# Performance work log

Measured on AMD Instinct MI355X. Metric: run time of the kernel, lower is better.

The kernel has to match this reference:

```python
import jax, jax.numpy as jnp
import numpy as np

NUM_HEADS = 8
EPS = 1e-5


def setup_inputs() -> dict:
    key = jax.random.key(0)
    ks = jax.random.split(key, 7)
    B, C, H, W, D = 1, 256, 16, 16, 16
    return {
        "x": jax.random.normal(ks[0], (B, C, H, W, D), dtype=jnp.float32),
        "w_dw": jax.random.normal(ks[1], (C, 1, 3, 3, 3), dtype=jnp.float32) * 0.05,
        "b_dw": jax.random.normal(ks[2], (C,), dtype=jnp.float32) * 0.05,
        "w_qkv": jax.random.normal(ks[3], (3 * C, C), dtype=jnp.float32) * 0.05,
        "b_qkv": jax.random.normal(ks[4], (3 * C,), dtype=jnp.float32) * 0.05,
        "w_proj": jax.random.normal(ks[5], (C, C), dtype=jnp.float32) * 0.05,
        "b_proj": jax.random.normal(ks[6], (C,), dtype=jnp.float32) * 0.05,
    }


def reference(x, w_dw, b_dw, w_qkv, b_qkv, w_proj, b_proj):
    B, C, H, W, D = x.shape
    nh = NUM_HEADS
    hd = C // nh
    scale = hd ** (-0.5)
    N = H * W * D

    # depthwise 3x3x3 conv (groups=C), SAME padding
    y = jax.lax.conv_general_dilated(
        x, w_dw, window_strides=(1, 1, 1), padding="SAME",
        dimension_numbers=("NCHWD", "OIHWD", "NCHWD"),
        feature_group_count=C,
    ) + b_dw[None, :, None, None, None]

    # InstanceNorm3d (affine=False): normalize over spatial dims per (b, c)
    mu = y.mean(axis=(2, 3, 4), keepdims=True)
    var = y.var(axis=(2, 3, 4), keepdims=True)
    y = (y - mu) * jax.lax.rsqrt(var + EPS)

    # 1x1x1 conv -> 3*C channels
    qkv = jnp.einsum("bchwd,oc->bohwd", y, w_qkv) + b_qkv[None, :, None, None, None]

    # [B, 3, nh, hd, N] -> q, k, v each [B, nh, N, hd]
    qkv = qkv.reshape(B, 3, nh, hd, N)
    q, k, v = jnp.transpose(qkv, (1, 0, 2, 4, 3))

    attn = jax.nn.softmax(jnp.einsum("bhnd,bhmd->bhnm", q, k) * scale, axis=-1)
    out = jnp.einsum("bhnm,bhmd->bhnd", attn, v)  # [B, nh, N, hd]

    # transpose(-1, -2) then reshape to [B, C, H, W, D]
    out = jnp.transpose(out, (0, 1, 3, 2)).reshape(B, C, H, W, D)

    # output 1x1x1 projection
    out = jnp.einsum("bchwd,oc->bohwd", out, w_proj) + b_proj[None, :, None, None, None]
    return out
```

## Files before the change

### kernel.cpp

```cpp
#include <hip/hip_runtime.h>
#include <hip/hip_bf16.h>

#define NSP 4096
#define QSC2 0.25503486f

typedef __attribute__((ext_vector_type(8))) short bf16x8;
typedef __attribute__((ext_vector_type(4))) float f32x4;

__device__ __forceinline__ unsigned short f2bf(float f){
  union{float f;unsigned int u;}c; c.f=f;
  unsigned int r = c.u + 0x7fffu + ((c.u>>16)&1u);
  return (unsigned short)(r>>16);
}
__device__ __forceinline__ unsigned int pk2(float a, float b){
  __hip_bfloat162 p = __float22bfloat162_rn(make_float2(a, b));
  unsigned int r; __builtin_memcpy(&r, &p, 4); return r;
}
__device__ __forceinline__ ushort4 pk4(float a, float b, float c, float d){
  union { ushort4 u4; uint2 u2; } u;
  u.u2.x = pk2(a, b); u.u2.y = pk2(c, d);
  return u.u4;
}

__global__ __launch_bounds__(512) void k_dwconv(
    const float* __restrict__ x,
    const float* __restrict__ wdw,
    const float* __restrict__ bdw,
    unsigned short* __restrict__ ybn)
{
  const int c = blockIdx.x;
  const int tid = threadIdx.x;
  __shared__ float xs[4096];
  __shared__ float wsh[27];
  __shared__ float bsh;
  __shared__ float rs[8], rq[8];

  const float* xc = x + (size_t)c * NSP;
  for (int i = tid; i < 1024; i += 512) *(float4*)&xs[i*4] = ((const float4*)xc)[i];
  if (tid < 27) wsh[tid] = wdw[c*27 + tid];
  if (tid == 31) bsh = bdw[c];
  __syncthreads();

  float yv[8];
  float sum = 0.f, sumsq = 0.f;
  #pragma unroll
  for (int i = 0; i < 8; i++){
    const int n = (i << 9) + tid;
    const int h = n >> 8, w = (n >> 4) & 15, d = n & 15;
    float acc = bsh;
    #pragma unroll
    for (int kh = 0; kh < 3; kh++){
      const int hh = h + kh - 1;
      if ((unsigned)hh >= 16u) continue;
      #pragma unroll
      for (int kw = 0; kw < 3; kw++){
        const int ww = w + kw - 1;
        if ((unsigned)ww >= 16u) continue;
        #pragma unroll
        for (int kd = 0; kd < 3; kd++){
          const int dd = d + kd - 1;
          if ((unsigned)dd >= 16u) continue;
          acc += wsh[kh*9 + kw*3 + kd] * xs[(hh<<8) + (ww<<4) + dd];
        }
      }
    }
    yv[i] = acc; sum += acc; sumsq += acc*acc;
  }
  #pragma unroll
  for (int off = 32; off > 0; off >>= 1){
    sum   += __shfl_down(sum, off, 64);
    sumsq += __shfl_down(sumsq, off, 64);
  }
  const int wid = tid >> 6, lane = tid & 63;
  if (lane == 0){ rs[wid] = sum; rq[wid] = sumsq; }
  __syncthreads();
  float ts = 0.f, tq = 0.f;
  #pragma unroll
  for (int i = 0; i < 8; i++){ ts += rs[i]; tq += rq[i]; }
  const float mean = ts * (1.f/4096.f);
  const float var  = tq * (1.f/4096.f) - mean*mean;
  const float rinv = rsqrtf(var + 1e-5f);
  unsigned short* yo = ybn + (size_t)c * NSP;
  #pragma unroll
  for (int i = 0; i < 8; i++) yo[(i<<9) + tid] = f2bf((yv[i] - mean) * rinv);
}

__global__ __launch_bounds__(256) void k_trans(
    const unsigned short* __restrict__ ybn,
    unsigned short* __restrict__ ynT)
{
  __shared__ unsigned short T[64][72];
  const int tid = threadIdx.x;
  const int n0 = blockIdx.x * 64, c0 = blockIdx.y * 64;
  const int cl = tid >> 4, n4 = (tid & 15) * 4;
  #pragma unroll
  for (int i = 0; i < 4; i++){
    const int c = cl + i*16;
    const ushort4 v = *(const ushort4*)(ybn + (size_t)(c0 + c) * NSP + n0 + n4);
    T[n4+0][c] = v.x; T[n4+1][c] = v.y; T[n4+2][c] = v.z; T[n4+3][c] = v.w;
  }
  __syncthreads();
  const int nl = tid >> 2, s8 = (tid & 3) * 16;
  *(uint4*)(ynT + (size_t)(n0+nl)*256 + c0 + s8)     = *(const uint4*)&T[nl][s8];
  *(uint4*)(ynT + (size_t)(n0+nl)*256 + c0 + s8 + 8) = *(const uint4*)&T[nl][s8 + 8];
}

__global__ __launch_bounds__(256) void k_qkv(
    const float* __restrict__ wqkv,
    const float* __restrict__ bqkv,
    const unsigned short* __restrict__ ynT,
    unsigned short* __restrict__ qb, unsigned short* __restrict__ kb,
    unsigned short* __restrict__ vbt)
{
  __shared__ unsigned short Wb[64][264];
  const int tid = threadIdx.x;
  const int o0 = blockIdx.y * 64;
  const int n0 = blockIdx.x * 128;
  {
    const int row = tid & 63, part = tid >> 6;
    const float* src = wqkv + (size_t)(o0 + row) * 256 + part * 64;
    unsigned short* dst = &Wb[row][part*64];
    #pragma unroll
    for (int j = 0; j < 8; j++){
      const float4 a = ((const float4*)src)[2*j];
      const float4 b = ((const float4*)src)[2*j+1];
      *(ushort4*)&dst[j*8]     = pk4(a.x, a.y, a.z, a.w);
      *(ushort4*)&dst[j*8 + 4] = pk4(b.x, b.y, b.z, b.w);
    }
  }
  __syncthreads();

  const int w = tid >> 6, lane = tid & 63, quad = lane >> 4, cc = lane & 15;
  const int nbase = n0 + w*32;
  const bool isv = (o0 >= 512);
  f32x4 acc[2][4] = {};

  #pragma unroll
  for (int k = 0; k < 8; k++){
    const bf16x8 y0 = *(const bf16x8*)(ynT + (size_t)(nbase + cc)  * 256 + k*32 + quad*8);
    const bf16x8 y1 = *(const bf16x8*)(ynT + (size_t)(nbase+16+cc) * 256 + k*32 + quad*8);
    #pragma unroll
    for (int os = 0; os < 4; os++){
      const bf16x8 wf = *(const bf16x8*)&Wb[os*16 + cc][k*32 + quad*8];
      if (!isv){
        acc[0][os] = __builtin_amdgcn_mfma_f32_16x16x32_bf16(y0, wf, acc[0][os], 0, 0, 0);
        acc[1][os] = __builtin_amdgcn_mfma_f32_16x16x32_bf16(y1, wf, acc[1][os], 0, 0, 0);
      } else {
        acc[0][os] = __builtin_amdgcn_mfma_f32_16x16x32_bf16(wf, y0, acc[0][os], 0, 0, 0);
        acc[1][os] = __builtin_amdgcn_mfma_f32_16x16x32_bf16(wf, y1, acc[1][os], 0, 0, 0);
      }
    }
  }

  if (!isv){
    #pragma unroll
    for (int os = 0; os < 4; os++){
      const int o = o0 + os*16 + cc;
      const int g = o >> 8, hh = (o >> 5) & 7, dd = o & 31;
      const float bias = bqkv[o];
      const float sc = (g == 0) ? QSC2 : 1.f;
      unsigned short* dst = (g == 0) ? qb : kb;
      #pragma unroll
      for (int ns = 0; ns < 2; ns++){
        #pragma unroll
        for (int r = 0; r < 4; r++){
          const int n = nbase + ns*16 + quad*4 + r;
          dst[((size_t)hh * NSP + n) * 32 + dd] = f2bf((acc[ns][os][r] + bias) * sc);
        }
      }
    }
  } else {
    #pragma unroll
    for (int os = 0; os < 4; os++){
      #pragma unroll
      for (int r = 0; r < 4; r++){
        const int orow = o0 - 512 + os*16 + quad*4 + r;
        const float bias = bqkv[512 + orow];
        #pragma unroll
        for (int ns = 0; ns < 2; ns++){
          const int n = nbase + ns*16 + cc;
          vbt[(size_t)orow * NSP + n] = f2bf(acc[ns][os][r] + bias);
        }
      }
    }
  }
}

__global__ __launch_bounds__(256) void k_attn(
    const unsigned short* __restrict__ qb,
    const unsigned short* __restrict__ kb,
    const unsigned short* __restrict__ vbt,
    float* __restrict__ op, float* __restrict__ lp)
{
  const int h = blockIdx.y, q0 = blockIdx.x * 64, z = blockIdx.z;
  const int tid = threadIdx.x;
  const int w = tid >> 6, lane = tid & 63, quad = lane >> 4, cc = lane & 15;

  __shared__ unsigned short ks [128][40];
  __shared__ unsigned short vsT[32][136];
  __shared__ unsigned short pst[64][136];

  const bf16x8 qf = *(const bf16x8*)(qb + ((size_t)(h * NSP + q0 + w*16 + cc)) * 32 + quad*8);
  const unsigned short* kbase = kb  + (size_t)h * NSP * 32;
  const unsigned short* vbase = vbt + (size_t)h * 32 * NSP;

  f32x4 o0 = {0.f,0.f,0.f,0.f}, o1 = {0.f,0.f,0.f,0.f};
  float lsum = 0.f;

  const int kt0 = z << 11;
  const int krow = tid >> 1, kseg = (tid & 1) * 16;
  const int vd = tid >> 3,  vseg = (tid & 7) * 16;

  for (int it = 0; it < 16; it++){
    const int kt = kt0 + it * 128;
    {
      const uint4* src = (const uint4*)(kbase + (size_t)(kt + krow) * 32 + kseg);
      const uint4 a = src[0], b = src[1];
      *(uint4*)&ks[krow][kseg]     = a;
      *(uint4*)&ks[krow][kseg + 8] = b;
    }
    {
      const uint4* src = (const uint4*)(vbase + (size_t)vd * NSP + kt + vseg);
      const uint4 a = src[0], b = src[1];
      *(uint4*)&vsT[vd][vseg]     = a;
      *(uint4*)&vsT[vd][vseg + 8] = b;
    }
    __syncthreads();

    #pragma unroll
    for (int t = 0; t < 8; t++){
      const bf16x8 kf = *(const bf16x8*)&ks[t*16 + cc][quad*8];
      f32x4 a = {0.f,0.f,0.f,0.f};
      a = __builtin_amdgcn_mfma_f32_16x16x32_bf16(kf, qf, a, 0, 0, 0);
      const float p0 = exp2f(a.x), p1 = exp2f(a.y);
      const float p2 = exp2f(a.z), p3 = exp2f(a.w);
      lsum += (p0 + p1) + (p2 + p3);
      *(ushort4*)&pst[w*16 + cc][t*16 + quad*4] = pk4(p0, p1, p2, p3);
    }
    #pragma unroll
    for (int ch = 0; ch < 4; ch++){
      const bf16x8 pf = *(const bf16x8*)&pst[w*16 + cc][ch*32 + quad*8];
      const bf16x8 va = *(const bf16x8*)&vsT[cc]     [ch*32 + quad*8];
      const bf16x8 vb = *(const bf16x8*)&vsT[16 + cc][ch*32 + quad*8];
      o0 = __builtin_amdgcn_mfma_f32_16x16x32_bf16(va, pf, o0, 0, 0, 0);
      o1 = __builtin_amdgcn_mfma_f32_16x16x32_bf16(vb, pf, o1, 0, 0, 0);
    }
    __syncthreads();
  }

  lsum += __shfl_xor(lsum, 16, 64);
  lsum += __shfl_xor(lsum, 32, 64);

  const int n = q0 + w*16 + cc;
  float* dst = op + ((size_t)z * NSP + n) * 256 + h*32;
  *(f32x4*)(dst + quad*4)      = o0;
  *(f32x4*)(dst + 16 + quad*4) = o1;
  if (quad == 0) lp[(size_t)z * 8 * NSP + h * NSP + n] = lsum;
}

__global__ __launch_bounds__(256) void k_proj(
    const float* __restrict__ wproj,
    const float* __restrict__ bproj,
    const float* __restrict__ op,
    const float* __restrict__ lp,
    float* __restrict__ out)
{
  __shared__ unsigned short Wb[64][264];
  const int tid = threadIdx.x;
  const int o0 = blockIdx.y * 64;
  const int n0 = blockIdx.x * 128;
  {
    const int row = tid & 63, part = tid >> 6;
    const float* src = wproj + (size_t)(o0 + row) * 256 + part * 64;
    unsigned short* dst = &Wb[row][part*64];
    #pragma unroll
    for (int j = 0; j < 8; j++){
      const float4 a = ((const float4*)src)[2*j];
      const float4 b = ((const float4*)src)[2*j+1];
      *(ushort4*)&dst[j*8]     = pk4(a.x, a.y, a.z, a.w);
      *(ushort4*)&dst[j*8 + 4] = pk4(b.x, b.y, b.z, b.w);
    }
  }
  __syncthreads();

  const int w = tid >> 6, lane = tid & 63, quad = lane >> 4, cc = lane & 15;
  const int nbase = n0 + w*32;
  f32x4 acc[2][4] = {};

  #pragma unroll
  for (int k = 0; k < 8; k++){
    const int n0r = nbase + cc, n1r = nbase + 16 + cc;
    const float r0 = 1.f / (lp[(size_t)k*NSP + n0r] + lp[(size_t)(8+k)*NSP + n0r]);
    const float r1 = 1.f / (lp[(size_t)k*NSP + n1r] + lp[(size_t)(8+k)*NSP + n1r]);
    const float* pa0 = op + (size_t)n0r * 256 + k*32 + quad*8;
    const float* pb0 = op + (size_t)(NSP + n0r) * 256 + k*32 + quad*8;
    const float* pa1 = op + (size_t)n1r * 256 + k*32 + quad*8;
    const float* pb1 = op + (size_t)(NSP + n1r) * 256 + k*32 + quad*8;
    const float4 a0 = ((const float4*)pa0)[0], a1 = ((const float4*)pa0)[1];
    const float4 b0 = ((const float4*)pb0)[0], b1 = ((const float4*)pb0)[1];
    const float4 c0 = ((const float4*)pa1)[0], c1 = ((const float4*)pa1)[1];
    const float4 d0 = ((const float4*)pb1)[0], d1 = ((const float4*)pb1)[1];
    union { bf16x8 v; ushort4 u[2]; } y0u, y1u;
    y0u.u[0] = pk4((a0.x+b0.x)*r0, (a0.y+b0.y)*r0, (a0.z+b0.z)*r0, (a0.w+b0.w)*r0);
    y0u.u[1] = pk4((a1.x+b1.x)*r0, (a1.y+b1.y)*r0, (a1.z+b1.z)*r0, (a1.w+b1.w)*r0);
    y1u.u[0] = pk4((c0.x+d0.x)*r1, (c0.y+d0.y)*r1, (c0.z+d0.z)*r1, (c0.w+d0.w)*r1);
    y1u.u[1] = pk4((c1.x+d1.x)*r1, (c1.y+d1.y)*r1, (c1.z+d1.z)*r1, (c1.w+d1.w)*r1);
    #pragma unroll
    for (int os = 0; os < 4; os++){
      const bf16x8 wf = *(const bf16x8*)&Wb[os*16 + cc][k*32 + quad*8];
      acc[0][os] = __builtin_amdgcn_mfma_f32_16x16x32_bf16(wf, y0u.v, acc[0][os], 0, 0, 0);
      acc[1][os] = __builtin_amdgcn_mfma_f32_16x16x32_bf16(wf, y1u.v, acc[1][os], 0, 0, 0);
    }
  }

  #pragma unroll
  for (int os = 0; os < 4; os++){
    #pragma unroll
    for (int r = 0; r < 4; r++){
      const int o = o0 + os*16 + quad*4 + r;
      const float bias = bproj[o];
      #pragma unroll
      for (int ns = 0; ns < 2; ns++){
        const int n = nbase + ns*16 + cc;
        out[(size_t)o * NSP + n] = acc[ns][os][r] + bias;
      }
    }
  }
}

extern "C" void kernel_launch(void* const* d_in, const int* in_sizes, int n_in,
                              void* d_out, int out_size, void* d_ws, size_t ws_size,
                              hipStream_t stream) {
  (void)in_sizes; (void)n_in; (void)out_size; (void)ws_size;
  const float* x     = (const float*)d_in[0];
  const float* wdw   = (const float*)d_in[1];
  const float* bdw   = (const float*)d_in[2];
  const float* wqkv  = (const float*)d_in[3];
  const float* bqkv  = (const float*)d_in[4];
  const float* wproj = (const float*)d_in[5];
  const float* bproj = (const float*)d_in[6];
  float* out = (float*)d_out;

  char* ws = (char*)d_ws;
  float*          op  = (float*)ws;
  unsigned short* ybn = (unsigned short*)ws;
  unsigned short* ynT = (unsigned short*)(ws + (2<<20));
  unsigned short* qb  = (unsigned short*)(ws + (8<<20));
  unsigned short* kb  = (unsigned short*)(ws + (10<<20));
  unsigned short* vbt = (unsigned short*)(ws + (12<<20));
  float*          lp  = (float*)(ws + (14<<20));

  k_dwconv <<<dim3(256),      dim3(512), 0, stream>>>(x, wdw, bdw, ybn);
  k_trans  <<<dim3(64, 4),    dim3(256), 0, stream>>>(ybn, ynT);
  k_qkv    <<<dim3(32, 12),   dim3(256), 0, stream>>>(wqkv, bqkv, ynT, qb, kb, vbt);
  k_attn   <<<dim3(64, 8, 2), dim3(256), 0, stream>>>(qb, kb, vbt, op, lp);
  k_proj   <<<dim3(32, 4),    dim3(256), 0, stream>>>(wproj, bproj, op, lp, out);
}
```

Baseline: 161.8 us.

## Use 32x32 MFMA in attention, shrink blocks, and split keys four ways

The attention kernel moves from 16x16x32 to 32x32x16 bf16 MFMAs, with each wave handling 32 queries. Blocks shrink to 128 threads and 64-key tiles. The key dimension is split into 4 partitions instead of 2 when the workspace is large enough, and the projection kernel now loops over the partial outputs and sums to combine them. The aim is more parallelism and higher MFMA throughput per instruction. The cost is more partial-result traffic through op/lp and more synchronisation steps per key tile.

After: 168.1 us. +3.9%, slower.

```diff
diff --git a/kernel.cpp b/kernel.cpp
--- a/kernel.cpp
+++ b/kernel.cpp
@@ -6,6 +6,7 @@
 
 typedef __attribute__((ext_vector_type(8))) short bf16x8;
 typedef __attribute__((ext_vector_type(4))) float f32x4;
+typedef __attribute__((ext_vector_type(16))) float f32x16;
 
 __device__ __forceinline__ unsigned short f2bf(float f){
   union{float f;unsigned int u;}c; c.f=f;
@@ -186,76 +187,82 @@
   }
 }
 
-__global__ __launch_bounds__(256) void k_attn(
+__global__ __launch_bounds__(128) void k_attn(
     const unsigned short* __restrict__ qb,
     const unsigned short* __restrict__ kb,
     const unsigned short* __restrict__ vbt,
-    float* __restrict__ op, float* __restrict__ lp)
+    float* __restrict__ op, float* __restrict__ lp, int ktlen)
 {
   const int h = blockIdx.y, q0 = blockIdx.x * 64, z = blockIdx.z;
   const int tid = threadIdx.x;
-  const int w = tid >> 6, lane = tid & 63, quad = lane >> 4, cc = lane & 15;
-
-  __shared__ unsigned short ks [128][40];
-  __shared__ unsigned short vsT[32][136];
-  __shared__ unsigned short pst[64][136];
-
-  const bf16x8 qf = *(const bf16x8*)(qb + ((size_t)(h * NSP + q0 + w*16 + cc)) * 32 + quad*8);
+  const int w = tid >> 6, l = tid & 63;
+  const int lq = l & 31, lb = l >> 5;
+
+  __shared__ unsigned short ks [64][40];
+  __shared__ unsigned short vsT[32][72];
+  __shared__ unsigned short pst[64][72];
+
+  const int qg = q0 + w*32 + lq;
+  const bf16x8 qf0 = *(const bf16x8*)(qb + ((size_t)(h*NSP + qg))*32 + lb*8);
+  const bf16x8 qf1 = *(const bf16x8*)(qb + ((size_t)(h*NSP + qg))*32 + 16 + lb*8);
   const unsigned short* kbase = kb  + (size_t)h * NSP * 32;
   const unsigned short* vbase = vbt + (size_t)h * 32 * NSP;
 
-  f32x4 o0 = {0.f,0.f,0.f,0.f}, o1 = {0.f,0.f,0.f,0.f};
+  f32x16 oacc = {};
   float lsum = 0.f;
 
-  const int kt0 = z << 11;
+  const int kt0 = z * ktlen;
   const int krow = tid >> 1, kseg = (tid & 1) * 16;
-  const int vd = tid >> 3,  vseg = (tid & 7) * 16;
-
-  for (int it = 0; it < 16; it++){
-    const int kt = kt0 + it * 128;
+  const int vrow = tid >> 2, vseg = (tid & 3) * 16;
+  const int iters = ktlen >> 6;
+
+  for (int it = 0; it < iters; it++){
+    const int kt = kt0 + it * 64;
     {
       const uint4* src = (const uint4*)(kbase + (size_t)(kt + krow) * 32 + kseg);
       const uint4 a = src[0], b = src[1];
       *(uint4*)&ks[krow][kseg]     = a;
       *(uint4*)&ks[krow][kseg + 8] = b;
-    }
-    {
-      const uint4* src = (const uint4*)(vbase + (size_t)vd * NSP + kt + vseg);
-      const uint4 a = src[0], b = src[1];
-      *(uint4*)&vsT[vd][vseg]     = a;
-      *(uint4*)&vsT[vd][vseg + 8] = b;
+      const uint4* vs = (const uint4*)(vbase + (size_t)vrow * NSP + kt + vseg);
+      const uint4 c = vs[0], d = vs[1];
+      *(uint4*)&vsT[vrow][vseg]     = c;
+      *(uint4*)&vsT[vrow][vseg + 8] = d;
     }
     __syncthreads();
 
     #pragma unroll
-    for (int t = 0; t < 8; t++){
-      const bf16x8 kf = *(const bf16x8*)&ks[t*16 + cc][quad*8];
-      f32x4 a = {0.f,0.f,0.f,0.f};
-      a = __builtin_amdgcn_mfma_f32_16x16x32_bf16(kf, qf, a, 0, 0, 0);
-      const float p0 = exp2f(a.x), p1 = exp2f(a.y);
-      const float p2 = exp2f(a.z), p3 = exp2f(a.w);
-      lsum += (p0 + p1) + (p2 + p3);
-      *(ushort4*)&pst[w*16 + cc][t*16 + quad*4] = pk4(p0, p1, p2, p3);
-    }
-    #pragma unroll
-    for (int ch = 0; ch < 4; ch++){
-      const bf16x8 pf = *(const bf16x8*)&pst[w*16 + cc][ch*32 + quad*8];
-      const bf16x8 va = *(const bf16x8*)&vsT[cc]     [ch*32 + quad*8];
-      const bf16x8 vb = *(const bf16x8*)&vsT[16 + cc][ch*32 + quad*8];
-      o0 = __builtin_amdgcn_mfma_f32_16x16x32_bf16(va, pf, o0, 0, 0, 0);
-      o1 = __builtin_amdgcn_mfma_f32_16x16x32_bf16(vb, pf, o1, 0, 0, 0);
+    for (int t2 = 0; t2 < 2; t2++){
+      const bf16x8 af0 = *(const bf16x8*)&ks[t2*32 + lq][lb*8];
+      const bf16x8 af1 = *(const bf16x8*)&ks[t2*32 + lq][16 + lb*8];
+      f32x16 sa = {};
+      sa = __builtin_amdgcn_mfma_f32_32x32x16_bf16(af0, qf0, sa, 0, 0, 0);
+      sa = __builtin_amdgcn_mfma_f32_32x32x16_bf16(af1, qf1, sa, 0, 0, 0);
+      #pragma unroll
+      for (int g = 0; g < 4; g++){
+        const float p0 = exp2f(sa[g*4+0]), p1 = exp2f(sa[g*4+1]);
+        const float p2 = exp2f(sa[g*4+2]), p3 = exp2f(sa[g*4+3]);
+        lsum += (p0 + p1) + (p2 + p3);
+        *(ushort4*)&pst[w*32 + lq][t2*32 + g*8 + lb*4] = pk4(p0, p1, p2, p3);
+      }
+    }
+    #pragma unroll
+    for (int ck = 0; ck < 4; ck++){
+      const bf16x8 vf = *(const bf16x8*)&vsT[lq]       [ck*16 + lb*8];
+      const bf16x8 pf = *(const bf16x8*)&pst[w*32 + lq][ck*16 + lb*8];
+      oacc = __builtin_amdgcn_mfma_f32_32x32x16_bf16(vf, pf, oacc, 0, 0, 0);
     }
     __syncthreads();
   }
 
-  lsum += __shfl_xor(lsum, 16, 64);
   lsum += __shfl_xor(lsum, 32, 64);
 
-  const int n = q0 + w*16 + cc;
-  float* dst = op + ((size_t)z * NSP + n) * 256 + h*32;
-  *(f32x4*)(dst + quad*4)      = o0;
-  *(f32x4*)(dst + 16 + quad*4) = o1;
-  if (quad == 0) lp[(size_t)z * 8 * NSP + h * NSP + n] = lsum;
+  float* dst = op + ((size_t)z * NSP + qg) * 256 + h*32;
+  #pragma unroll
+  for (int g = 0; g < 4; g++){
+    f32x4 v = { oacc[g*4+0], oacc[g*4+1], oacc[g*4+2], oacc[g*4+3] };
+    *(f32x4*)(dst + g*8 + lb*4) = v;
+  }
+  if (lb == 0) lp[((size_t)z * 8 + h) * NSP + qg] = lsum;
 }
 
 __global__ __launch_bounds__(256) void k_proj(
@@ -263,7 +270,7 @@
     const float* __restrict__ bproj,
     const float* __restrict__ op,
     const float* __restrict__ lp,
-    float* __restrict__ out)
+    float* __restrict__ out, int nz)
 {
   __shared__ unsigned short Wb[64][264];
   const int tid = threadIdx.x;
@@ -290,21 +297,22 @@
   #pragma unroll
   for (int k = 0; k < 8; k++){
     const int n0r = nbase + cc, n1r = nbase + 16 + cc;
-    const float r0 = 1.f / (lp[(size_t)k*NSP + n0r] + lp[(size_t)(8+k)*NSP + n0r]);
-    const float r1 = 1.f / (lp[(size_t)k*NSP + n1r] + lp[(size_t)(8+k)*NSP + n1r]);
-    const float* pa0 = op + (size_t)n0r * 256 + k*32 + quad*8;
-    const float* pb0 = op + (size_t)(NSP + n0r) * 256 + k*32 + quad*8;
-    const float* pa1 = op + (size_t)n1r * 256 + k*32 + quad*8;
-    const float* pb1 = op + (size_t)(NSP + n1r) * 256 + k*32 + quad*8;
-    const float4 a0 = ((const float4*)pa0)[0], a1 = ((const float4*)pa0)[1];
-    const float4 b0 = ((const float4*)pb0)[0], b1 = ((const float4*)pb0)[1];
-    const float4 c0 = ((const float4*)pa1)[0], c1 = ((const float4*)pa1)[1];
-    const float4 d0 = ((const float4*)pb1)[0], d1 = ((const float4*)pb1)[1];
+    float l0 = 0.f, l1 = 0.f;
+    f32x4 s00 = {}, s01 = {}, s10 = {}, s11 = {};
+    for (int z = 0; z < nz; z++){
+      l0 += lp[((size_t)z*8 + k) * NSP + n0r];
+      l1 += lp[((size_t)z*8 + k) * NSP + n1r];
+      const float* p0 = op + ((size_t)z * NSP + n0r) * 256 + k*32 + quad*8;
+      const float* p1 = op + ((size_t)z * NSP + n1r) * 256 + k*32 + quad*8;
+      s00 += *(const f32x4*)p0;  s01 += *(const f32x4*)(p0 + 4);
+      s10 += *(const f32x4*)p1;  s11 += *(const f32x4*)(p1 + 4);
+    }
+    const float r0 = 1.f / l0, r1 = 1.f / l1;
     union { bf16x8 v; ushort4 u[2]; } y0u, y1u;
-    y0u.u[0] = pk4((a0.x+b0.x)*r0, (a0.y+b0.y)*r0, (a0.z+b0.z)*r0, (a0.w+b0.w)*r0);
-    y0u.u[1] = pk4((a1.x+b1.x)*r0, (a1.y+b1.y)*r0, (a1.z+b1.z)*r0, (a1.w+b1.w)*r0);
-    y1u.u[0] = pk4((c0.x+d0.x)*r1, (c0.y+d0.y)*r1, (c0.z+d0.z)*r1, (c0.w+d0.w)*r1);
-    y1u.u[1] = pk4((c1.x+d1.x)*r1, (c1.y+d1.y)*r1, (c1.z+d1.z)*r1, (c1.w+d1.w)*r1);
+    y0u.u[0] = pk4(s00[0]*r0, s00[1]*r0, s00[2]*r0, s00[3]*r0);
+    y0u.u[1] = pk4(s01[0]*r0, s01[1]*r0, s01[2]*r0, s01[3]*r0);
+    y1u.u[0] = pk4(s10[0]*r1, s10[1]*r1, s10[2]*r1, s10[3]*r1);
+    y1u.u[1] = pk4(s11[0]*r1, s11[1]*r1, s11[2]*r1, s11[3]*r1);
     #pragma unroll
     for (int os = 0; os < 4; os++){
       const bf16x8 wf = *(const bf16x8*)&Wb[os*16 + cc][k*32 + quad*8];
@@ -331,7 +339,7 @@
 extern "C" void kernel_launch(void* const* d_in, const int* in_sizes, int n_in,
                               void* d_out, int out_size, void* d_ws, size_t ws_size,
                               hipStream_t stream) {
-  (void)in_sizes; (void)n_in; (void)out_size; (void)ws_size;
+  (void)in_sizes; (void)n_in; (void)out_size;
   const float* x     = (const float*)d_in[0];
   const float* wdw   = (const float*)d_in[1];
   const float* bdw   = (const float*)d_in[2];
@@ -341,18 +349,22 @@
   const float* bproj = (const float*)d_in[6];
   float* out = (float*)d_out;
 
+  const int nz = (ws_size >= ((size_t)24 << 20)) ? 4 : 2;
+  const int ktlen = NSP / nz;
+
   char* ws = (char*)d_ws;
+  const size_t opB = (size_t)nz << 22;
   float*          op  = (float*)ws;
   unsigned short* ybn = (unsigned short*)ws;
   unsigned short* ynT = (unsigned short*)(ws + (2<<20));
-  unsigned short* qb  = (unsigned short*)(ws + (8<<20));
-  unsigned short* kb  = (unsigned short*)(ws + (10<<20));
-  unsigned short* vbt = (unsigned short*)(ws + (12<<20));
-  float*          lp  = (float*)(ws + (14<<20));
-
-  k_dwconv <<<dim3(256),      dim3(512), 0, stream>>>(x, wdw, bdw, ybn);
-  k_trans  <<<dim3(64, 4),    dim3(256), 0, stream>>>(ybn, ynT);
-  k_qkv    <<<dim3(32, 12),   dim3(256), 0, stream>>>(wqkv, bqkv, ynT, qb, kb, vbt);
-  k_attn   <<<dim3(64, 8, 2), dim3(256), 0, stream>>>(qb, kb, vbt, op, lp);
-  k_proj   <<<dim3(32, 4),    dim3(256), 0, stream>>>(wproj, bproj, op, lp, out);
-}
+  unsigned short* qb  = (unsigned short*)(ws + opB);
+  unsigned short* kb  = (unsigned short*)(ws + opB + (2<<20));
+  unsigned short* vbt = (unsigned short*)(ws + opB + (4<<20));
+  float*          lp  = (float*)(ws + opB + (6<<20));
+
+  k_dwconv <<<dim3(256),        dim3(512), 0, stream>>>(x, wdw, bdw, ybn);
+  k_trans  <<<dim3(64, 4),      dim3(256), 0, stream>>>(ybn, ynT);
+  k_qkv    <<<dim3(32, 12),     dim3(256), 0, stream>>>(wqkv, bqkv, ynT, qb, kb, vbt);
+  k_attn   <<<dim3(64, 8, nz),  dim3(128), 0, stream>>>(qb, kb, vbt, op, lp, ktlen);
+  k_proj   <<<dim3(32, 4),      dim3(256), 0, stream>>>(wproj, bproj, op, lp, out, nz);
+}
```
